# Optimization experiments

Hardware: AMD Instinct MI355X
Metric: run time of the kernel (lower is better)

The kernel has to match this reference:

```python
import jax, jax.numpy as jnp
import numpy as np

LATENT, D_MODEL, WIN, ENC_IN, BATCH = 128, 512, 256, 55, 256


def setup_inputs() -> dict:
    key = jax.random.key(0)
    ks = jax.random.split(key, 9)
    sl = lambda k, shape, fan_in: (jax.random.normal(k, shape, jnp.float32) / np.sqrt(fan_in)).astype(jnp.float32)
    return {
        "z": jax.random.normal(ks[0], (BATCH, LATENT), jnp.float32),
        "h_proj_w": sl(ks[1], (D_MODEL, LATENT), LATENT),
        "h_proj_b": sl(ks[2], (D_MODEL,), LATENT),
        "w_ih": sl(ks[3], (3 * D_MODEL, D_MODEL), D_MODEL),
        "w_hh": sl(ks[4], (3 * D_MODEL, D_MODEL), D_MODEL),
        "b_ih": sl(ks[5], (3 * D_MODEL,), D_MODEL),
        "b_hh": sl(ks[6], (3 * D_MODEL,), D_MODEL),
        "out_w": sl(ks[7], (ENC_IN, D_MODEL), D_MODEL),
        "out_b": sl(ks[8], (ENC_IN,), D_MODEL),
        "win_size": WIN,
    }


def reference(z, h_proj_w, h_proj_b, w_ih, w_hh, b_ih, b_hh, out_w, out_b, win_size):
    d = h_proj_w.shape[0]
    # h0 = tanh(Linear(z)) -> [B, d]
    h0 = jnp.tanh(z @ h_proj_w.T + h_proj_b)
    # GRU input is all zeros, so input-gate preactivation is just b_ih
    # (w_ih @ 0 == 0); gate order in torch GRU is (r, z, n).
    gi_r, gi_z, gi_n = b_ih[:d], b_ih[d:2 * d], b_ih[2 * d:]

    def step(h, _):
        gh = h @ w_hh.T + b_hh                      # [B, 3d]
        r = jax.nn.sigmoid(gi_r + gh[:, :d])
        zg = jax.nn.sigmoid(gi_z + gh[:, d:2 * d])
        n = jnp.tanh(gi_n + r * gh[:, 2 * d:])
        h_new = (1.0 - zg) * n + zg * h
        return h_new, h_new

    _, hs = jax.lax.scan(step, h0, None, length=win_size)  # [T, B, d]
    hs = jnp.transpose(hs, (1, 0, 2))                      # [B, T, d]
    return hs @ out_w.T + out_b                            # [B, T, enc_in]
```

## Files before the change

### kernel.cpp

```cpp
#include <hip/hip_runtime.h>

#define DM     512
#define LAT    128
#define WIN_   256
#define ENC    55
#define GB     32
#define BT     8
#define DS     64
#define TPB    768
#define OUT_T  256
#define AROW16 528
#define GHS    200
#define OWS    520
#define NK     22
#define NKP    24

typedef __attribute__((ext_vector_type(8))) short bf8;
typedef __attribute__((ext_vector_type(4))) float f4;
typedef unsigned long long u64;
typedef unsigned short u16;

__device__ __align__(128) u64 g_ring2[2][GB][8][BT][NKP];
__device__ __align__(128) u64 g_lcnt[GB * 8 * 16];

__device__ __forceinline__ u16 f2bf(float f) {
    union { float f; unsigned int i; } v; v.f = f;
    unsigned int r = v.i + 0x7fffu + ((v.i >> 16) & 1u);
    return (u16)(r >> 16);
}
__device__ __forceinline__ float sigm(float x) { return 1.f / (1.f + __expf(-x)); }
__device__ __forceinline__ float tanh_(float x) {
    x = fminf(x, 40.f);
    float e = __expf(2.f * x);
    return (e - 1.f) / (e + 1.f);
}
#define ALOAD(p)     __hip_atomic_load((p),      __ATOMIC_RELAXED, __HIP_MEMORY_SCOPE_AGENT)
#define ASTORE(p, v) __hip_atomic_store((p), (v), __ATOMIC_RELAXED, __HIP_MEMORY_SCOPE_AGENT)

__global__ __launch_bounds__(TPB, 3) void gru_fused(
    const float* __restrict__ z,
    const float* __restrict__ hpw,
    const float* __restrict__ hpb,
    const float* __restrict__ whh,
    const float* __restrict__ bih,
    const float* __restrict__ bhh,
    const float* __restrict__ outw,
    const float* __restrict__ outb,
    float* __restrict__ out)
{
    const int blk  = blockIdx.x;
    const int g    = blk & (GB - 1);
    const int s    = blk >> 5;
    const int d0   = s * DS;
    const int row0 = g * BT;
    const int tid  = threadIdx.x;
    const int wave = tid >> 6;
    const int lane = tid & 63;
    const int quad = lane >> 4;
    const int nl   = lane & 15;

    __shared__ __align__(16) u16 sm16[BT * AROW16];
    __shared__ __align__(16) float ghT[BT][GHS];
    __shared__ float bias_r[DS], bias_z[DS], gin_[DS], bhn_[DS];
    __shared__ __align__(16) u16 hpack[BT][66];
    __shared__ __align__(16) u16 sOutW[ENC * OWS];
    __shared__ float sOutB[64];
    __shared__ u64 sh_lc;

    u64* lc_own = g_lcnt + (u64)(g * 8 + s) * 16;
    if (tid == 0) sh_lc = ALOAD(lc_own);

    if (tid < DS) {
        int dg = d0 + tid;
        bias_r[tid] = bih[dg]       + bhh[dg];
        bias_z[tid] = bih[512 + dg] + bhh[512 + dg];
        gin_[tid]   = bih[1024 + dg];
        bhn_[tid]   = bhh[1024 + dg];
    }
    if (tid < ENC) sOutB[tid] = outb[tid];
    for (int i = tid; i < ENC * DM; i += TPB)
        sOutW[(i >> 9) * OWS + (i & 511)] = f2bf(outw[i]);

    const int gl   = wave * 16 + nl;
    const int sel  = gl >> 6;
    const int jrow = sel * 512 + d0 + (gl & 63);
    bf8 bfrag[16];
#pragma unroll
    for (int kb = 0; kb < 16; ++kb) {
        const float* wp = whh + jrow * DM + kb * 32 + quad * 8;
        bf8 v;
#pragma unroll
        for (int j = 0; j < 8; ++j) v[j] = (short)f2bf(wp[j]);
        bfrag[kb] = v;
    }
    __syncthreads();

    const u64 base = sh_lc * 512ULL + 1ULL;
    float hprev_reg = 0.f;

    if (wave < BT) {
        float acc = hpb[d0 + lane];
        const float* zr = z + (row0 + wave) * LAT;
        const float* wr = hpw + (d0 + lane) * LAT;
#pragma unroll 8
        for (int k = 0; k < LAT; ++k) acc += zr[k] * wr[k];
        hprev_reg = tanh_(acc);
        if (lane < 2) hpack[wave][64 + lane] = 0;
        hpack[wave][lane] = f2bf(hprev_reg);
        const u16 sq = (u16)base;
        if (lane < NK) {
            u16 b0 = hpack[wave][3 * lane], b1 = hpack[wave][3 * lane + 1],
                b2 = hpack[wave][3 * lane + 2];
            u64 rec = (u64)sq | ((u64)b0 << 16) | ((u64)b1 << 32) | ((u64)b2 << 48);
            ASTORE(&g_ring2[0][g][s][wave][lane], rec);
        }
    }

    const u16* afrag_base = sm16 + (nl & 7) * AROW16;

    for (int t = 1; t <= WIN_; ++t) {
        const int sp = (t - 1) & 1, sc = t & 1;
        const u16 want = (u16)(base + t - 1);

        if (wave < BT) {
            sm16[wave * AROW16 + d0 + lane] = f2bf(hprev_reg);
        }
        if (wave >= 1 && wave < 8) {
            const int j = (s + wave) & 7;
            const u64* rb = &g_ring2[sp][g][j][0][0];
            const int row = lane >> 3, k = lane & 7;
            {
                const u64* pp = rb + 7 * NKP + 21;
                long guard = 0;
                while ((u16)ALOAD(pp) != want && guard < (1L << 18)) ++guard;
            }
            const u64* p0 = rb + row * NKP + k;
            const bool v2 = (k + 16) < NK;
            u64 r0 = ALOAD(p0), r1 = ALOAD(p0 + 8), r2 = v2 ? ALOAD(p0 + 16) : 0;
            bool ok0 = ((u16)r0 == want), ok1 = ((u16)r1 == want),
                 ok2 = (!v2) || ((u16)r2 == want);
            long guard = 0;
            while (!__all(ok0 && ok1 && ok2) && guard < (1L << 18)) {
                if (!ok0) { r0 = ALOAD(p0);      ok0 = ((u16)r0 == want); }
                if (!ok1) { r1 = ALOAD(p0 + 8);  ok1 = ((u16)r1 == want); }
                if (!ok2) { r2 = ALOAD(p0 + 16); ok2 = ((u16)r2 == want); }
                ++guard;
            }
            u16* dst = sm16 + row * AROW16 + j * 64;
            int db = 3 * k;
            dst[db] = (u16)(r0 >> 16); dst[db + 1] = (u16)(r0 >> 32); dst[db + 2] = (u16)(r0 >> 48);
            db = 3 * (k + 8);
            dst[db] = (u16)(r1 >> 16); dst[db + 1] = (u16)(r1 >> 32); dst[db + 2] = (u16)(r1 >> 48);
            if (v2) {
                db = 3 * (k + 16);
                dst[db] = (u16)(r2 >> 16);
                if (db + 1 < DS) dst[db + 1] = (u16)(r2 >> 32);
                if (db + 2 < DS) dst[db + 2] = (u16)(r2 >> 48);
            }
        }
        __syncthreads();

        f4 acc = {0.f, 0.f, 0.f, 0.f};
#pragma unroll
        for (int kb = 0; kb < 16; ++kb) {
            bf8 av = *(const bf8*)(afrag_base + quad * 8 + kb * 32);
            acc = __builtin_amdgcn_mfma_f32_16x16x32_bf16(av, bfrag[kb], acc, 0, 0, 0);
        }
        if (quad < 2) {
#pragma unroll
            for (int r = 0; r < 4; ++r) ghT[quad * 4 + r][gl] = acc[r];
        }
        __syncthreads();

        if (wave < BT) {
            const int d = lane;
            const float* grow = &ghT[wave][0];
            float rr = sigm(bias_r[d] + grow[d]);
            float zg = sigm(bias_z[d] + grow[64 + d]);
            float nn = tanh_(gin_[d] + rr * (bhn_[d] + grow[128 + d]));
            float h  = (1.f - zg) * nn + zg * hprev_reg;
            hprev_reg = h;
            hpack[wave][d] = f2bf(h);
            const u16 sq = (u16)(base + t);
            if (lane < NK) {
                u16 b0 = hpack[wave][3 * lane], b1 = hpack[wave][3 * lane + 1],
                    b2 = hpack[wave][3 * lane + 2];
                u64 rec = (u64)sq | ((u64)b0 << 16) | ((u64)b1 << 32) | ((u64)b2 << 48);
                ASTORE(&g_ring2[sc][g][s][wave][lane], rec);
            }
        }

        const int tau = t - 2;
        const bool proj = (tau >= 0) && ((tau & 7) == s);
        if (proj && wave >= 8) {
            const int e  = (wave - 8) * 16 + nl;
            const int ec = (e < ENC) ? e : (ENC - 1);
            const u16* wrow = sOutW + ec * OWS + quad * 8;
            f4 accp = {0.f, 0.f, 0.f, 0.f};
#pragma unroll
            for (int kb = 0; kb < 16; ++kb) {
                bf8 av = *(const bf8*)(afrag_base + quad * 8 + kb * 32);
                bf8 wv = *(const bf8*)(wrow + kb * 32);
                accp = __builtin_amdgcn_mfma_f32_16x16x32_bf16(av, wv, accp, 0, 0, 0);
            }
            if (quad < 2 && e < ENC) {
                float ob = sOutB[e];
#pragma unroll
                for (int r = 0; r < 4; ++r) {
                    int m = quad * 4 + r;
                    out[(row0 + m) * (OUT_T * ENC) + tau * ENC + e] = accp[r] + ob;
                }
            }
        }
        if (proj) __syncthreads();
    }

    if (s == 7) {
        const u16 want = (u16)(base + WIN_);
        if (wave < BT)
            sm16[wave * AROW16 + d0 + lane] = f2bf(hprev_reg);
        if (wave >= 1 && wave < 8) {
            const int j = (s + wave) & 7;
            const u64* rb = &g_ring2[0][g][j][0][0];
            const int row = lane >> 3, k = lane & 7;
            {
                const u64* pp = rb + 7 * NKP + 21;
                long guard = 0;
                while ((u16)ALOAD(pp) != want && guard < (1L << 18)) ++guard;
            }
            const u64* p0 = rb + row * NKP + k;
            const bool v2 = (k + 16) < NK;
            u64 r0 = ALOAD(p0), r1 = ALOAD(p0 + 8), r2 = v2 ? ALOAD(p0 + 16) : 0;
            bool ok0 = ((u16)r0 == want), ok1 = ((u16)r1 == want),
                 ok2 = (!v2) || ((u16)r2 == want);
            long guard = 0;
            while (!__all(ok0 && ok1 && ok2) && guard < (1L << 18)) {
                if (!ok0) { r0 = ALOAD(p0);      ok0 = ((u16)r0 == want); }
                if (!ok1) { r1 = ALOAD(p0 + 8);  ok1 = ((u16)r1 == want); }
                if (!ok2) { r2 = ALOAD(p0 + 16); ok2 = ((u16)r2 == want); }
                ++guard;
            }
            u16* dst = sm16 + row * AROW16 + j * 64;
            int db = 3 * k;
            dst[db] = (u16)(r0 >> 16); dst[db + 1] = (u16)(r0 >> 32); dst[db + 2] = (u16)(r0 >> 48);
            db = 3 * (k + 8);
            dst[db] = (u16)(r1 >> 16); dst[db + 1] = (u16)(r1 >> 32); dst[db + 2] = (u16)(r1 >> 48);
            if (v2) {
                db = 3 * (k + 16);
                dst[db] = (u16)(r2 >> 16);
                if (db + 1 < DS) dst[db + 1] = (u16)(r2 >> 32);
                if (db + 2 < DS) dst[db + 2] = (u16)(r2 >> 48);
            }
        }
        __syncthreads();
        if (wave >= 8) {
            const int e  = (wave - 8) * 16 + nl;
            const int ec = (e < ENC) ? e : (ENC - 1);
            const u16* wrow = sOutW + ec * OWS + quad * 8;
            f4 accp = {0.f, 0.f, 0.f, 0.f};
#pragma unroll
            for (int kb = 0; kb < 16; ++kb) {
                bf8 av = *(const bf8*)(afrag_base + quad * 8 + kb * 32);
                bf8 wv = *(const bf8*)(wrow + kb * 32);
                accp = __builtin_amdgcn_mfma_f32_16x16x32_bf16(av, wv, accp, 0, 0, 0);
            }
            if (quad < 2 && e < ENC) {
                float ob = sOutB[e];
#pragma unroll
                for (int r = 0; r < 4; ++r) {
                    int m = quad * 4 + r;
                    out[(row0 + m) * (OUT_T * ENC) + 255 * ENC + e] = accp[r] + ob;
                }
            }
        }
    }

    if (tid == 0) ASTORE(lc_own, sh_lc + 1ULL);
}

extern "C" void kernel_launch(void* const* d_in, const int* in_sizes, int n_in,
                              void* d_out, int out_size, void* d_ws, size_t ws_size,
                              hipStream_t stream) {
    const float* z    = (const float*)d_in[0];
    const float* hpw  = (const float*)d_in[1];
    const float* hpb  = (const float*)d_in[2];
    const float* whh  = (const float*)d_in[4];
    const float* bih  = (const float*)d_in[5];
    const float* bhh  = (const float*)d_in[6];
    const float* outw = (const float*)d_in[7];
    const float* outb = (const float*)d_in[8];
    float* out = (float*)d_out;

    (void)d_ws; (void)ws_size;
    gru_fused<<<dim3(256), dim3(TPB), 0, stream>>>(
        z, hpw, hpb, whh, bih, bhh, outw, outb, out);
}
```

Measured before the change: 698.5 us.

## Split hidden dimension across 4 blocks per batch group instead of 8

```diff
diff --git a/kernel.cpp b/kernel.cpp
--- a/kernel.cpp
+++ b/kernel.cpp
@@ -5,22 +5,23 @@
 #define WIN_   256
 #define ENC    55
 #define GB     32
+#define NSL    4
+#define DSL    128
 #define BT     8
-#define DS     64
 #define TPB    768
 #define OUT_T  256
 #define AROW16 528
-#define GHS    200
+#define GH2    392
 #define OWS    520
-#define NK     22
-#define NKP    24
+#define NK     43
+#define NKP    44
 
 typedef __attribute__((ext_vector_type(8))) short bf8;
 typedef __attribute__((ext_vector_type(4))) float f4;
 typedef unsigned long long u64;
 typedef unsigned short u16;
 
-__device__ __align__(128) u64 g_ring2[2][GB][8][BT][NKP];
+__device__ __align__(128) u64 g_ring2[2][GB][NSL][BT][NKP];
 __device__ __align__(128) u64 g_lcnt[GB * 8 * 16];
 
 __device__ __forceinline__ u16 f2bf(float f) {
@@ -51,7 +52,7 @@
     const int blk  = blockIdx.x;
     const int g    = blk & (GB - 1);
     const int s    = blk >> 5;
-    const int d0   = s * DS;
+    const int d0   = s * DSL;
     const int row0 = g * BT;
     const int tid  = threadIdx.x;
     const int wave = tid >> 6;
@@ -60,17 +61,17 @@
     const int nl   = lane & 15;
 
     __shared__ __align__(16) u16 sm16[BT * AROW16];
-    __shared__ __align__(16) float ghT[BT][GHS];
-    __shared__ float bias_r[DS], bias_z[DS], gin_[DS], bhn_[DS];
-    __shared__ __align__(16) u16 hpack[BT][66];
+    __shared__ __align__(16) float ghT[BT][GH2];
+    __shared__ float bias_r[DSL], bias_z[DSL], gin_[DSL], bhn_[DSL];
+    __shared__ __align__(16) u16 hpack[BT][132];
     __shared__ __align__(16) u16 sOutW[ENC * OWS];
     __shared__ float sOutB[64];
     __shared__ u64 sh_lc;
 
-    u64* lc_own = g_lcnt + (u64)(g * 8 + s) * 16;
+    u64* lc_own = g_lcnt + (u64)(g * 4 + s) * 16;
     if (tid == 0) sh_lc = ALOAD(lc_own);
 
-    if (tid < DS) {
+    if (tid < DSL) {
         int dg = d0 + tid;
         bias_r[tid] = bih[dg]       + bhh[dg];
         bias_z[tid] = bih[512 + dg] + bhh[512 + dg];
@@ -81,32 +82,36 @@
     for (int i = tid; i < ENC * DM; i += TPB)
         sOutW[(i >> 9) * OWS + (i & 511)] = f2bf(outw[i]);
 
-    const int gl   = wave * 16 + nl;
-    const int sel  = gl >> 6;
-    const int jrow = sel * 512 + d0 + (gl & 63);
-    bf8 bfrag[16];
+    const int lr0 = wave * 16 + nl;
+    const int lr1 = lr0 + 192;
+    const int jrow0 = (lr0 >> 7) * 512 + d0 + (lr0 & 127);
+    const int jrow1 = (lr1 >> 7) * 512 + d0 + (lr1 & 127);
+    bf8 bfragA[16], bfragB[16];
 #pragma unroll
     for (int kb = 0; kb < 16; ++kb) {
-        const float* wp = whh + jrow * DM + kb * 32 + quad * 8;
-        bf8 v;
-#pragma unroll
-        for (int j = 0; j < 8; ++j) v[j] = (short)f2bf(wp[j]);
-        bfrag[kb] = v;
+        const float* wpA = whh + jrow0 * DM + kb * 32 + quad * 8;
+        const float* wpB = whh + jrow1 * DM + kb * 32 + quad * 8;
+        bf8 va, vb;
+#pragma unroll
+        for (int j = 0; j < 8; ++j) { va[j] = (short)f2bf(wpA[j]); vb[j] = (short)f2bf(wpB[j]); }
+        bfragA[kb] = va; bfragB[kb] = vb;
     }
     __syncthreads();
 
     const u64 base = sh_lc * 512ULL + 1ULL;
-    float hprev_reg = 0.f;
+    float hprev0 = 0.f, hprev1 = 0.f;
 
     if (wave < BT) {
-        float acc = hpb[d0 + lane];
         const float* zr = z + (row0 + wave) * LAT;
-        const float* wr = hpw + (d0 + lane) * LAT;
+        float a0 = hpb[d0 + lane], a1 = hpb[d0 + 64 + lane];
+        const float* w0 = hpw + (d0 + lane) * LAT;
+        const float* w1 = hpw + (d0 + 64 + lane) * LAT;
 #pragma unroll 8
-        for (int k = 0; k < LAT; ++k) acc += zr[k] * wr[k];
-        hprev_reg = tanh_(acc);
-        if (lane < 2) hpack[wave][64 + lane] = 0;
-        hpack[wave][lane] = f2bf(hprev_reg);
+        for (int k = 0; k < LAT; ++k) { float zv = zr[k]; a0 += zv * w0[k]; a1 += zv * w1[k]; }
+        hprev0 = tanh_(a0); hprev1 = tanh_(a1);
+        if (lane < 4) hpack[wave][128 + lane] = 0;
+        hpack[wave][lane]      = f2bf(hprev0);
+        hpack[wave][64 + lane] = f2bf(hprev1);
         const u16 sq = (u16)base;
         if (lane < NK) {
             u16 b0 = hpack[wave][3 * lane], b1 = hpack[wave][3 * lane + 1],
@@ -123,64 +128,82 @@
         const u16 want = (u16)(base + t - 1);
 
         if (wave < BT) {
-            sm16[wave * AROW16 + d0 + lane] = f2bf(hprev_reg);
-        }
-        if (wave >= 1 && wave < 8) {
-            const int j = (s + wave) & 7;
+            sm16[wave * AROW16 + d0 + lane]      = f2bf(hprev0);
+            sm16[wave * AROW16 + d0 + 64 + lane] = f2bf(hprev1);
+        }
+        if (wave >= 1 && wave < 4) {
+            const int j = (s + wave) & 3;
             const u64* rb = &g_ring2[sp][g][j][0][0];
-            const int row = lane >> 3, k = lane & 7;
+            const int row = lane >> 3, kb2 = lane & 7;
             {
-                const u64* pp = rb + 7 * NKP + 21;
+                const u64* pp = rb + 7 * NKP + 42;
                 long guard = 0;
                 while ((u16)ALOAD(pp) != want && guard < (1L << 18)) ++guard;
             }
-            const u64* p0 = rb + row * NKP + k;
-            const bool v2 = (k + 16) < NK;
-            u64 r0 = ALOAD(p0), r1 = ALOAD(p0 + 8), r2 = v2 ? ALOAD(p0 + 16) : 0;
-            bool ok0 = ((u16)r0 == want), ok1 = ((u16)r1 == want),
-                 ok2 = (!v2) || ((u16)r2 == want);
+            const u64* p0 = rb + row * NKP + kb2;
+            u64 r[6]; bool ok[6];
+#pragma unroll
+            for (int i = 0; i < 6; ++i) {
+                bool v = (kb2 + 8 * i) < NK;
+                r[i] = v ? ALOAD(p0 + 8 * i) : 0;
+                ok[i] = (!v) || ((u16)r[i] == want);
+            }
             long guard = 0;
-            while (!__all(ok0 && ok1 && ok2) && guard < (1L << 18)) {
-                if (!ok0) { r0 = ALOAD(p0);      ok0 = ((u16)r0 == want); }
-                if (!ok1) { r1 = ALOAD(p0 + 8);  ok1 = ((u16)r1 == want); }
-                if (!ok2) { r2 = ALOAD(p0 + 16); ok2 = ((u16)r2 == want); }
+            while (!__all(ok[0] && ok[1] && ok[2] && ok[3] && ok[4] && ok[5]) &&
+                   guard < (1L << 18)) {
+#pragma unroll
+                for (int i = 0; i < 6; ++i)
+                    if (!ok[i]) { r[i] = ALOAD(p0 + 8 * i); ok[i] = ((u16)r[i] == want); }
                 ++guard;
             }
-            u16* dst = sm16 + row * AROW16 + j * 64;
-            int db = 3 * k;
-            dst[db] = (u16)(r0 >> 16); dst[db + 1] = (u16)(r0 >> 32); dst[db + 2] = (u16)(r0 >> 48);
-            db = 3 * (k + 8);
-            dst[db] = (u16)(r1 >> 16); dst[db + 1] = (u16)(r1 >> 32); dst[db + 2] = (u16)(r1 >> 48);
-            if (v2) {
-                db = 3 * (k + 16);
-                dst[db] = (u16)(r2 >> 16);
-                if (db + 1 < DS) dst[db + 1] = (u16)(r2 >> 32);
-                if (db + 2 < DS) dst[db + 2] = (u16)(r2 >> 48);
+            u16* dst = sm16 + row * AROW16 + j * DSL;
+#pragma unroll
+            for (int i = 0; i < 6; ++i) {
+                int k = kb2 + 8 * i;
+                if (k < NK) {
+                    int dd = 3 * k;
+                    dst[dd] = (u16)(r[i] >> 16);
+                    if (dd + 1 < DSL) dst[dd + 1] = (u16)(r[i] >> 32);
+                    if (dd + 2 < DSL) dst[dd + 2] = (u16)(r[i] >> 48);
+                }
             }
         }
         __syncthreads();
 
-        f4 acc = {0.f, 0.f, 0.f, 0.f};
+        f4 acc0 = {0.f, 0.f, 0.f, 0.f}, acc1 = {0.f, 0.f, 0.f, 0.f};
 #pragma unroll
         for (int kb = 0; kb < 16; ++kb) {
             bf8 av = *(const bf8*)(afrag_base + quad * 8 + kb * 32);
-            acc = __builtin_amdgcn_mfma_f32_16x16x32_bf16(av, bfrag[kb], acc, 0, 0, 0);
+            acc0 = __builtin_amdgcn_mfma_f32_16x16x32_bf16(av, bfragA[kb], acc0, 0, 0, 0);
+            acc1 = __builtin_amdgcn_mfma_f32_16x16x32_bf16(av, bfragB[kb], acc1, 0, 0, 0);
         }
         if (quad < 2) {
 #pragma unroll
-            for (int r = 0; r < 4; ++r) ghT[quad * 4 + r][gl] = acc[r];
+            for (int r = 0; r < 4; ++r) {
+                ghT[quad * 4 + r][lr0]       = acc0[r];
+                ghT[quad * 4 + r][lr0 + 192] = acc1[r];
+            }
         }
         __syncthreads();
 
         if (wave < BT) {
-            const int d = lane;
             const float* grow = &ghT[wave][0];
-            float rr = sigm(bias_r[d] + grow[d]);
-            float zg = sigm(bias_z[d] + grow[64 + d]);
-            float nn = tanh_(gin_[d] + rr * (bhn_[d] + grow[128 + d]));
-            float h  = (1.f - zg) * nn + zg * hprev_reg;
-            hprev_reg = h;
-            hpack[wave][d] = f2bf(h);
+            {
+                const int d = lane;
+                float rr = sigm(bias_r[d] + grow[d]);
+                float zg = sigm(bias_z[d] + grow[128 + d]);
+                float nn = tanh_(gin_[d] + rr * (bhn_[d] + grow[256 + d]));
+                hprev0 = (1.f - zg) * nn + zg * hprev0;
+                hpack[wave][d] = f2bf(hprev0);
+            }
+            {
+                const int d = 64 + lane;
+                float rr = sigm(bias_r[d] + grow[d]);
+                float zg = sigm(bias_z[d] + grow[128 + d]);
+                float nn = tanh_(gin_[d] + rr * (bhn_[d] + grow[256 + d]));
+                hprev1 = (1.f - zg) * nn + zg * hprev1;
+                hpack[wave][d] = f2bf(hprev1);
+            }
             const u16 sq = (u16)(base + t);
             if (lane < NK) {
                 u16 b0 = hpack[wave][3 * lane], b1 = hpack[wave][3 * lane + 1],
@@ -191,7 +214,7 @@
         }
 
         const int tau = t - 2;
-        const bool proj = (tau >= 0) && ((tau & 7) == s);
+        const bool proj = (tau >= 0) && ((tau & 3) == s);
         if (proj && wave >= 8) {
             const int e  = (wave - 8) * 16 + nl;
             const int ec = (e < ENC) ? e : (ENC - 1);
@@ -215,41 +238,47 @@
         if (proj) __syncthreads();
     }
 
-    if (s == 7) {
+    if (s == 3) {
         const u16 want = (u16)(base + WIN_);
-        if (wave < BT)
-            sm16[wave * AROW16 + d0 + lane] = f2bf(hprev_reg);
-        if (wave >= 1 && wave < 8) {
-            const int j = (s + wave) & 7;
+        if (wave < BT) {
+            sm16[wave * AROW16 + d0 + lane]      = f2bf(hprev0);
+            sm16[wave * AROW16 + d0 + 64 + lane] = f2bf(hprev1);
+        }
+        if (wave >= 1 && wave < 4) {
+            const int j = (s + wave) & 3;
             const u64* rb = &g_ring2[0][g][j][0][0];
-            const int row = lane >> 3, k = lane & 7;
+            const int row = lane >> 3, kb2 = lane & 7;
             {
-                const u64* pp = rb + 7 * NKP + 21;
+                const u64* pp = rb + 7 * NKP + 42;
                 long guard = 0;
                 while ((u16)ALOAD(pp) != want && guard < (1L << 18)) ++guard;
             }
-            const u64* p0 = rb + row * NKP + k;
-            const bool v2 = (k + 16) < NK;
-            u64 r0 = ALOAD(p0), r1 = ALOAD(p0 + 8), r2 = v2 ? ALOAD(p0 + 16) : 0;
-            bool ok0 = ((u16)r0 == want), ok1 = ((u16)r1 == want),
-                 ok2 = (!v2) || ((u16)r2 == want);
+            const u64* p0 = rb + row * NKP + kb2;
+            u64 r[6]; bool ok[6];
+#pragma unroll
+            for (int i = 0; i < 6; ++i) {
+                bool v = (kb2 + 8 * i) < NK;
+                r[i] = v ? ALOAD(p0 + 8 * i) : 0;
+                ok[i] = (!v) || ((u16)r[i] == want);
+            }
             long guard = 0;
-            while (!__all(ok0 && ok1 && ok2) && guard < (1L << 18)) {
-                if (!ok0) { r0 = ALOAD(p0);      ok0 = ((u16)r0 == want); }
-                if (!ok1) { r1 = ALOAD(p0 + 8);  ok1 = ((u16)r1 == want); }
-                if (!ok2) { r2 = ALOAD(p0 + 16); ok2 = ((u16)r2 == want); }
+            while (!__all(ok[0] && ok[1] && ok[2] && ok[3] && ok[4] && ok[5]) &&
+                   guard < (1L << 18)) {
+#pragma unroll
+                for (int i = 0; i < 6; ++i)
+                    if (!ok[i]) { r[i] = ALOAD(p0 + 8 * i); ok[i] = ((u16)r[i] == want); }
                 ++guard;
             }
-            u16* dst = sm16 + row * AROW16 + j * 64;
-            int db = 3 * k;
-            dst[db] = (u16)(r0 >> 16); dst[db + 1] = (u16)(r0 >> 32); dst[db + 2] = (u16)(r0 >> 48);
-            db = 3 * (k + 8);
-            dst[db] = (u16)(r1 >> 16); dst[db + 1] = (u16)(r1 >> 32); dst[db + 2] = (u16)(r1 >> 48);
-            if (v2) {
-                db = 3 * (k + 16);
-                dst[db] = (u16)(r2 >> 16);
-                if (db + 1 < DS) dst[db + 1] = (u16)(r2 >> 32);
-                if (db + 2 < DS) dst[db + 2] = (u16)(r2 >> 48);
+            u16* dst = sm16 + row * AROW16 + j * DSL;
+#pragma unroll
+            for (int i = 0; i < 6; ++i) {
+                int k = kb2 + 8 * i;
+                if (k < NK) {
+                    int dd = 3 * k;
+                    dst[dd] = (u16)(r[i] >> 16);
+                    if (dd + 1 < DSL) dst[dd + 1] = (u16)(r[i] >> 32);
+                    if (dd + 2 < DSL) dst[dd + 2] = (u16)(r[i] >> 48);
+                }
             }
         }
         __syncthreads();
@@ -292,6 +321,6 @@
     float* out = (float*)d_out;
 
     (void)d_ws; (void)ws_size;
-    gru_fused<<<dim3(256), dim3(TPB), 0, stream>>>(
+    gru_fused<<<dim3(128), dim3(TPB), 0, stream>>>(
         z, hpw, hpb, whh, bih, bhh, outw, outb, out);
 }
```

New measurement: 1.306 ms. +87.0%, slower.
